# Performance work log

Measured on AMD Instinct MI355X. Metric: run time of the kernel, lower is better.

## Reference

```python
import jax, jax.numpy as jnp
import numpy as np

B, N, E, C_IN, C_OUT = 16, 4096, 131072, 256, 256


def setup_inputs() -> dict:
    key = jax.random.key(0)
    k1, k2, k3, k4 = jax.random.split(key, 4)
    x = jax.random.normal(k1, (B, N, C_IN), dtype=jnp.float32)
    edge_index = jax.random.randint(k2, (B, 2, E), 0, N, dtype=jnp.int32)
    edge_weight = jax.random.uniform(k3, (B, E), dtype=jnp.float32)
    # glorot init for weight [C_in, C_out]
    scale = float(np.sqrt(6.0 / (C_IN + C_OUT)))
    W = jax.random.uniform(k4, (C_IN, C_OUT), dtype=jnp.float32, minval=-scale, maxval=scale)
    return {"x": x, "edge_index": edge_index, "edge_weight": edge_weight, "W": W}


def _gcn_one_graph(xi, ei, ewi, W):
    # xi: [N, C_in], ei: [2, E+N], ewi: [E+N]
    n = xi.shape[0]
    row, col = ei[0], ei[1]
    deg = jax.ops.segment_sum(ewi, row, num_segments=n)            # [N]
    deg_inv = jnp.where(deg > 0, jax.lax.rsqrt(deg), 0.0)          # deg^-0.5, inf -> 0
    norm = deg_inv[row] * ewi * deg_inv[col]                       # [E+N]
    xw = xi @ W                                                    # [N, C_out]
    msg = norm[:, None] * xw[col]                                  # gather + scale
    out = jax.ops.segment_sum(msg, row, num_segments=n)            # scatter-add to rows
    return jax.nn.relu(out)                                        # act = F.relu, bias=False


def reference(x, edge_index, edge_weight, W):
    b, n, _ = x.shape
    # add self loops with weight 1 (fill_value=1)
    loop = jnp.arange(n, dtype=edge_index.dtype)
    loop_idx = jnp.broadcast_to(jnp.stack([loop, loop])[None], (b, 2, n))
    ei = jnp.concatenate([edge_index, loop_idx], axis=-1)          # [B, 2, E+N]
    ew = jnp.concatenate([edge_weight, jnp.ones((b, n), x.dtype)], axis=-1)  # [B, E+N]
    return jax.vmap(_gcn_one_graph, in_axes=(0, 0, 0, None))(x, ei, ew, W)
```

## Files before the change

### kernel.cpp

```cpp
#include <hip/hip_runtime.h>
#include <cstdint>
#include <cstddef>

#define BB 16
#define NN 4096
#define EE 131072
#define CIN 256
#define COUT 256
#define NCH 16
#define CHE (EE / NCH)

typedef __attribute__((ext_vector_type(8))) _Float16 h16x8;
typedef __attribute__((ext_vector_type(4))) float f32x4;

__global__ __launch_bounds__(256) void phaseA_kernel(const float* __restrict__ W, _Float16* __restrict__ wt,
                                                     const int* __restrict__ ei, const float* __restrict__ ew,
                                                     int* __restrict__ chist, float* __restrict__ wdeg) {
    __shared__ int h[NN];
    __shared__ float wh[NN];
    int bid = blockIdx.x;
    int tid = threadIdx.x;
    if (bid < BB * NCH) {
        int b = bid >> 4, c = bid & (NCH - 1);
        for (int i = tid; i < NN; i += 256) { h[i] = 0; wh[i] = 0.f; }
        __syncthreads();
        const int* rows = ei + (size_t)b * 2 * EE + (size_t)c * CHE;
        const float* w = ew + (size_t)b * EE + (size_t)c * CHE;
        #pragma unroll 4
        for (int j = 0; j < CHE / 256; ++j) {
            int row = rows[j * 256 + tid];
            float wv = w[j * 256 + tid];
            atomicAdd(&h[row], 1);
            atomicAdd(&wh[row], wv);
        }
        __syncthreads();
        int* co = chist + ((size_t)b * NCH + c) * NN;
        float* wo = wdeg + ((size_t)b * NCH + c) * NN;
        for (int i = tid; i < NN; i += 256) { co[i] = h[i]; wo[i] = wh[i]; }
    } else {
        int n = bid - BB * NCH;
        int k = tid;
        wt[n * CIN + k] = (_Float16)W[(size_t)k * COUT + n];
    }
}

__global__ __launch_bounds__(1024) void scanfused_kernel(const int* __restrict__ chist, const float* __restrict__ wdeg,
                                                         int* __restrict__ chunkbase, int* __restrict__ roff,
                                                         float* __restrict__ dinv) {
    int b = blockIdx.x, tid = threadIdx.x;
    int wid = tid >> 6, lane = tid & 63;
    __shared__ int wsum[16];
    __shared__ int wbase[16];
    __shared__ int gtot_s;
    int carry = 0;
    for (int g = 0; g < 4; ++g) {
        int r = g * 1024 + tid;
        int cv[NCH];
        int tot = 0;
        float dsum = 1.0f;
        #pragma unroll
        for (int c = 0; c < NCH; ++c) {
            size_t idx = ((size_t)b * NCH + c) * NN + r;
            cv[c] = chist[idx];
            tot += cv[c];
            dsum += wdeg[idx];
        }
        dinv[b * NN + r] = rsqrtf(dsum);
        int incl = tot;
        #pragma unroll
        for (int off = 1; off < 64; off <<= 1) {
            int t = __shfl_up(incl, off, 64);
            if (lane >= off) incl += t;
        }
        if (lane == 63) wsum[wid] = incl;
        __syncthreads();
        if (wid == 0) {
            int v = (lane < 16) ? wsum[lane] : 0;
            int winc = v;
            #pragma unroll
            for (int off = 1; off < 16; off <<= 1) {
                int t = __shfl_up(winc, off, 64);
                if (lane >= off) winc += t;
            }
            if (lane < 16) wbase[lane] = winc - v;
            if (lane == 15) gtot_s = winc;
        }
        __syncthreads();
        int excl = carry + wbase[wid] + (incl - tot);
        roff[b * NN + r] = excl;
        int acc = excl;
        #pragma unroll
        for (int c = 0; c < NCH; ++c) {
            chunkbase[((size_t)b * NCH + c) * NN + r] = acc;
            acc += cv[c];
        }
        carry += gtot_s;
        __syncthreads();
    }
}

__global__ __launch_bounds__(256) void gemm_f32wide_kernel(const float* __restrict__ x, const _Float16* __restrict__ wt,
                                                           _Float16* __restrict__ xw) {
    __shared__ _Float16 As[128 * 64];
    __shared__ _Float16 Bs[256 * 64];
    int tid = threadIdx.x;
    int lane = tid & 63;
    int wave = tid >> 6;
    int row0 = blockIdx.x * 128;
    int wr = wave >> 1, wc = wave & 1;
    int hi = lane >> 4, lo = lane & 15;
    f32x4 acc[4][8] = {};

    for (int kk = 0; kk < CIN; kk += 64) {
        #pragma unroll
        for (int j = 0; j < 4; ++j) {
            int c = j * 256 + tid;
            int r = c >> 3, kq = c & 7;
            const float* g = &x[(size_t)(row0 + r) * CIN + kk + 8 * kq];
            float4 f0 = *reinterpret_cast<const float4*>(g);
            float4 f1 = *reinterpret_cast<const float4*>(g + 4);
            h16x8 v;
            v[0] = (_Float16)f0.x; v[1] = (_Float16)f0.y; v[2] = (_Float16)f0.z; v[3] = (_Float16)f0.w;
            v[4] = (_Float16)f1.x; v[5] = (_Float16)f1.y; v[6] = (_Float16)f1.z; v[7] = (_Float16)f1.w;
            *reinterpret_cast<h16x8*>(&As[r * 64 + 8 * kq]) = v;
        }
        #pragma unroll
        for (int j = 0; j < 8; ++j) {
            int c = j * 256 + tid;
            int r = c >> 3, kq = c & 7;
            *reinterpret_cast<h16x8*>(&Bs[r * 64 + 8 * kq]) =
                *reinterpret_cast<const h16x8*>(&wt[(size_t)r * CIN + kk + 8 * kq]);
        }
        __syncthreads();
        #pragma unroll
        for (int ks = 0; ks < 2; ++ks) {
            h16x8 a[4], b[8];
            #pragma unroll
            for (int m = 0; m < 4; ++m)
                a[m] = *reinterpret_cast<const h16x8*>(&As[(wr * 64 + m * 16 + lo) * 64 + ks * 32 + 8 * hi]);
            #pragma unroll
            for (int n = 0; n < 8; ++n)
                b[n] = *reinterpret_cast<const h16x8*>(&Bs[(wc * 128 + n * 16 + lo) * 64 + ks * 32 + 8 * hi]);
            #pragma unroll
            for (int m = 0; m < 4; ++m)
                #pragma unroll
                for (int n = 0; n < 8; ++n)
                    acc[m][n] = __builtin_amdgcn_mfma_f32_16x16x32_f16(a[m], b[n], acc[m][n], 0, 0, 0);
        }
        __syncthreads();
    }
    #pragma unroll
    for (int m = 0; m < 4; ++m)
        #pragma unroll
        for (int n = 0; n < 8; ++n)
            #pragma unroll
            for (int r = 0; r < 4; ++r) {
                int row = row0 + wr * 64 + m * 16 + hi * 4 + r;
                int col = wc * 128 + n * 16 + lo;
                xw[(size_t)row * COUT + col] = (_Float16)acc[m][n][r];
            }
}

__global__ __launch_bounds__(256) void scatter2_kernel(const int* __restrict__ ei, const float* __restrict__ ew,
                                                       const float* __restrict__ dinv, const int* __restrict__ chunkbase,
                                                       int2* __restrict__ csr) {
    __shared__ int basebuf[NN];
    __shared__ float dinvs[NN];
    int bid = blockIdx.x;
    int xcd = bid & 7;
    int j = bid >> 3;
    int b = xcd * 2 + (j >> 4);
    int c = j & (NCH - 1);
    int tid = threadIdx.x;
    for (int i = tid; i < NN; i += 256) {
        basebuf[i] = chunkbase[((size_t)b * NCH + c) * NN + i];
        dinvs[i] = dinv[b * NN + i];
    }
    __syncthreads();
    const int* rows = ei + (size_t)b * 2 * EE + (size_t)c * CHE;
    const int* cols = rows + EE;
    const float* w = ew + (size_t)b * EE + (size_t)c * CHE;
    int2* cs = csr + (size_t)b * EE;
    #pragma unroll 4
    for (int jj = 0; jj < CHE / 256; ++jj) {
        int e = jj * 256 + tid;
        int row = rows[e];
        int col = cols[e];
        float nm = dinvs[row] * w[e] * dinvs[col];
        int pos = atomicAdd(&basebuf[row], 1);
        int2 pk; pk.x = col * (COUT * 2); pk.y = __float_as_int(nm);
        cs[pos] = pk;
    }
}

#define MIXLO(acc_, w_, nm_) asm("v_fma_mix_f32 %0, %1, %2, %0 op_sel:[0,0,0] op_sel_hi:[1,0,0]" \
                                 : "+v"(acc_) : "v"(w_), "v"(nm_));
#define MIXHI(acc_, w_, nm_) asm("v_fma_mix_f32 %0, %1, %2, %0 op_sel:[1,0,0] op_sel_hi:[1,0,0]" \
                                 : "+v"(acc_) : "v"(w_), "v"(nm_));
#define ACCMIX(w_, nm_) { \
    MIXLO(a0, (w_).x, nm_); MIXHI(a1, (w_).x, nm_); \
    MIXLO(a2, (w_).y, nm_); MIXHI(a3, (w_).y, nm_); \
    MIXLO(a4, (w_).z, nm_); MIXHI(a5, (w_).z, nm_); \
    MIXLO(a6, (w_).w, nm_); MIXHI(a7, (w_).w, nm_); }

__global__ __launch_bounds__(256) void aggregate_kernel(const _Float16* __restrict__ xw, const float* __restrict__ dinv,
                                                        const int* __restrict__ roff, const int2* __restrict__ csr,
                                                        float* __restrict__ out) {
    int bid = blockIdx.x;
    int xcd = bid & 7;
    int idx = bid >> 3;
    int b = xcd * 2 + (idx >> 10);
    int rowblk = idx & 1023;
    int wave = threadIdx.x >> 6;
    int lane = threadIdx.x & 63;
    int n = rowblk * 4 + wave;
    bool hiHalf = lane >= 32;
    int sub = lane & 31;
    int lanebyte = sub * 16;

    const int* rb = roff + b * NN;
    int s = __builtin_amdgcn_readfirstlane(rb[n]);
    int eRaw = (n == NN - 1) ? EE : rb[n + 1];
    int e = __builtin_amdgcn_readfirstlane(eRaw);
    int cnt = e - s;
    const int2* cs = csr + (size_t)b * EE + s;

    const char* xwbase = (const char*)(xw + (size_t)b * NN * COUT);
    float a0 = 0.f, a1 = 0.f, a2 = 0.f, a3 = 0.f, a4 = 0.f, a5 = 0.f, a6 = 0.f, a7 = 0.f;

    {
        float di = dinv[b * NN + n];
        float sn = hiHalf ? 0.f : di * di;
        uint4 w = *reinterpret_cast<const uint4*>(xwbase + (size_t)n * (COUT * 2) + lanebyte);
        ACCMIX(w, sn);
    }

    int m = cnt & ~7;
    int i = 0;
    for (; i < m; i += 8) {
        int2 q[8];
        #pragma unroll
        for (int u = 0; u < 8; ++u) q[u] = cs[i + u];
        #pragma unroll
        for (int u = 0; u < 4; ++u) {
            int offx = (hiHalf ? q[2 * u + 1].x : q[2 * u].x) + lanebyte;
            float nm = __int_as_float(hiHalf ? q[2 * u + 1].y : q[2 * u].y);
            uint4 w = *reinterpret_cast<const uint4*>(xwbase + (uint32_t)offx);
            ACCMIX(w, nm);
        }
    }
    if (i < cnt) {
        #pragma unroll
        for (int u = 0; u < 4; ++u) {
            int j0 = i + 2 * u, j1 = j0 + 1;
            int jc0 = (j0 < cnt) ? j0 : cnt - 1;
            int jc1 = (j1 < cnt) ? j1 : cnt - 1;
            int2 q0 = cs[jc0];
            int2 q1 = cs[jc1];
            int offx = (hiHalf ? q1.x : q0.x) + lanebyte;
            float nm0 = (j0 < cnt) ? __int_as_float(q0.y) : 0.f;
            float nm1 = (j1 < cnt) ? __int_as_float(q1.y) : 0.f;
            float nm = hiHalf ? nm1 : nm0;
            uint4 w = *reinterpret_cast<const uint4*>(xwbase + (uint32_t)offx);
            ACCMIX(w, nm);
        }
    }

    a0 += __shfl(a0, lane ^ 32, 64); a1 += __shfl(a1, lane ^ 32, 64);
    a2 += __shfl(a2, lane ^ 32, 64); a3 += __shfl(a3, lane ^ 32, 64);
    a4 += __shfl(a4, lane ^ 32, 64); a5 += __shfl(a5, lane ^ 32, 64);
    a6 += __shfl(a6, lane ^ 32, 64); a7 += __shfl(a7, lane ^ 32, 64);

    float4 o = hiHalf
        ? make_float4(fmaxf(a4, 0.f), fmaxf(a5, 0.f), fmaxf(a6, 0.f), fmaxf(a7, 0.f))
        : make_float4(fmaxf(a0, 0.f), fmaxf(a1, 0.f), fmaxf(a2, 0.f), fmaxf(a3, 0.f));
    float* orow = out + ((size_t)b * NN + n) * COUT + sub * 8 + (hiHalf ? 4 : 0);
    *reinterpret_cast<float4*>(orow) = o;
}

__global__ __launch_bounds__(256) void cvt_wt_kernel(const float* __restrict__ W, _Float16* __restrict__ wt) {
    int n = blockIdx.x;
    int k = threadIdx.x;
    wt[n * CIN + k] = (_Float16)W[(size_t)k * COUT + n];
}

__global__ __launch_bounds__(256) void init_deg_kernel(float* __restrict__ deg, float v) {
    int i = blockIdx.x * 256 + threadIdx.x;
    if (i < BB * NN) deg[i] = v;
}

__global__ __launch_bounds__(256) void deg_only_kernel(const int* __restrict__ ei, const float* __restrict__ ew,
                                                       float* __restrict__ deg) {
    int idx = blockIdx.x * 256 + threadIdx.x;
    if (idx >= BB * EE) return;
    int b = idx / EE, e = idx - b * EE;
    atomicAdd(&deg[b * NN + ei[(size_t)b * 2 * EE + e]], ew[(size_t)b * EE + e]);
}

__global__ __launch_bounds__(256) void deginv_kernel(const float* __restrict__ deg, float* __restrict__ dinv) {
    int i = blockIdx.x * 256 + threadIdx.x;
    if (i < BB * NN) {
        float d = deg[i];
        dinv[i] = (d > 0.0f) ? rsqrtf(d) : 0.0f;
    }
}

__global__ __launch_bounds__(256) void gemm_f32src_kernel(const float* __restrict__ x, const _Float16* __restrict__ wt,
                                                          _Float16* __restrict__ xw) {
    __shared__ _Float16 As[128][64];
    __shared__ _Float16 Bs[128][64];
    int tid = threadIdx.x;
    int lane = tid & 63;
    int wave = tid >> 6;
    int row0 = blockIdx.x * 128;
    int col0 = blockIdx.y * 128;
    int wr = wave >> 1, wc = wave & 1;
    int hi = lane >> 4, lo = lane & 15;
    f32x4 acc[4][4] = {};
    for (int kk = 0; kk < CIN; kk += 64) {
        #pragma unroll
        for (int j = 0; j < 4; ++j) {
            int c = j * 256 + tid;
            int r = c >> 3, kq = c & 7;
            const float* g = &x[(size_t)(row0 + r) * CIN + kk + 8 * kq];
            float4 f0 = *reinterpret_cast<const float4*>(g);
            float4 f1 = *reinterpret_cast<const float4*>(g + 4);
            h16x8 v;
            v[0] = (_Float16)f0.x; v[1] = (_Float16)f0.y; v[2] = (_Float16)f0.z; v[3] = (_Float16)f0.w;
            v[4] = (_Float16)f1.x; v[5] = (_Float16)f1.y; v[6] = (_Float16)f1.z; v[7] = (_Float16)f1.w;
            *reinterpret_cast<h16x8*>(&As[r][8 * kq]) = v;
        }
        #pragma unroll
        for (int j = 0; j < 4; ++j) {
            int c = j * 256 + tid;
            int r = c >> 3, kq = c & 7;
            *reinterpret_cast<h16x8*>(&Bs[r][8 * kq]) =
                *reinterpret_cast<const h16x8*>(&wt[(size_t)(col0 + r) * CIN + kk + 8 * kq]);
        }
        __syncthreads();
        #pragma unroll
        for (int ks = 0; ks < 2; ++ks) {
            h16x8 a[4], b[4];
            #pragma unroll
            for (int m = 0; m < 4; ++m)
                a[m] = *reinterpret_cast<const h16x8*>(&As[wr * 64 + m * 16 + lo][ks * 32 + 8 * hi]);
            #pragma unroll
            for (int n = 0; n < 4; ++n)
                b[n] = *reinterpret_cast<const h16x8*>(&Bs[wc * 64 + n * 16 + lo][ks * 32 + 8 * hi]);
            #pragma unroll
            for (int m = 0; m < 4; ++m)
                #pragma unroll
                for (int n = 0; n < 4; ++n)
                    acc[m][n] = __builtin_amdgcn_mfma_f32_16x16x32_f16(a[m], b[n], acc[m][n], 0, 0, 0);
        }
        __syncthreads();
    }
    #pragma unroll
    for (int m = 0; m < 4; ++m)
        #pragma unroll
        for (int n = 0; n < 4; ++n)
            #pragma unroll
            for (int r = 0; r < 4; ++r) {
                int row = row0 + wr * 64 + m * 16 + hi * 4 + r;
                int col = col0 + wc * 64 + n * 16 + lo;
                xw[(size_t)row * COUT + col] = (_Float16)acc[m][n][r];
            }
}

__global__ __launch_bounds__(256) void self_kernel(const _Float16* __restrict__ xw, const float* __restrict__ dinv,
                                                   float* __restrict__ out) {
    int bn = blockIdx.x;
    int c = threadIdx.x;
    float di = dinv[bn];
    out[(size_t)bn * COUT + c] = di * di * (float)xw[(size_t)bn * COUT + c];
}

__global__ __launch_bounds__(256) void scatter_atomic_kernel(const int* __restrict__ ei, const float* __restrict__ ew,
                                                             const float* __restrict__ dinv,
                                                             const _Float16* __restrict__ xw, float* __restrict__ out) {
    int be = blockIdx.x;
    int b = be / EE, e = be - b * EE;
    int c = threadIdx.x;
    int row = ei[(size_t)b * 2 * EE + e];
    int col = ei[(size_t)b * 2 * EE + EE + e];
    float w = ew[(size_t)b * EE + e];
    float nm = dinv[b * NN + row] * w * dinv[b * NN + col];
    const _Float16* xwb = xw + (size_t)b * NN * COUT;
    atomicAdd(&out[((size_t)b * NN + row) * COUT + c], nm * (float)xwb[(size_t)col * COUT + c]);
}

__global__ __launch_bounds__(256) void relu_kernel(float* __restrict__ out) {
    size_t i = (size_t)blockIdx.x * 256 + threadIdx.x;
    out[i] = fmaxf(out[i], 0.0f);
}

extern "C" void kernel_launch(void* const* d_in, const int* in_sizes, int n_in,
                              void* d_out, int out_size, void* d_ws, size_t ws_size,
                              hipStream_t stream) {
    const float* x  = (const float*)d_in[0];
    const int*   ei = (const int*)d_in[1];
    const float* ew = (const float*)d_in[2];
    const float* Wm = (const float*)d_in[3];
    float* out = (float*)d_out;

    char* ws = (char*)d_ws;
    size_t off = 0;
    auto alloc = [&](size_t bytes) -> void* {
        void* p = ws + off;
        off += (bytes + 255) & ~(size_t)255;
        return p;
    };
    _Float16* xw        = (_Float16*)alloc((size_t)BB * NN * COUT * 2);
    int2*     csr       = (int2*)alloc((size_t)BB * EE * 8);
    int*      chist     = (int*)alloc((size_t)BB * NCH * NN * 4);
    float*    wdeg      = (float*)alloc((size_t)BB * NCH * NN * 4);
    int*      chunkbase = (int*)alloc((size_t)BB * NCH * NN * 4);
    int*      roff      = (int*)alloc((size_t)BB * NN * 4);
    float*    dinv      = (float*)alloc((size_t)BB * NN * 4);
    _Float16* wt        = (_Float16*)alloc((size_t)CIN * COUT * 2);
    float*    deg_fb    = (float*)chist;
    bool use_csr = (ws_size >= off);

    if (use_csr) {
        phaseA_kernel<<<BB * NCH + COUT, 256, 0, stream>>>(Wm, wt, ei, ew, chist, wdeg);
        scanfused_kernel<<<BB, 1024, 0, stream>>>(chist, wdeg, chunkbase, roff, dinv);
        gemm_f32wide_kernel<<<BB * NN / 128, 256, 0, stream>>>(x, wt, xw);
        scatter2_kernel<<<BB * NCH, 256, 0, stream>>>(ei, ew, dinv, chunkbase, csr);
        aggregate_kernel<<<BB * NN / 4, 256, 0, stream>>>(xw, dinv, roff, csr, out);
    } else {
        const int bnBlocks = (BB * NN) / 256;
        cvt_wt_kernel<<<COUT, CIN, 0, stream>>>(Wm, wt);
        init_deg_kernel<<<bnBlocks, 256, 0, stream>>>(deg_fb, 1.0f);
        deg_only_kernel<<<(BB * EE) / 256, 256, 0, stream>>>(ei, ew, deg_fb);
        deginv_kernel<<<bnBlocks, 256, 0, stream>>>(deg_fb, dinv);
        dim3 ggrid((BB * NN) / 128, COUT / 128);
        gemm_f32src_kernel<<<ggrid, 256, 0, stream>>>(x, wt, xw);
        self_kernel<<<BB * NN, 256, 0, stream>>>(xw, dinv, out);
        scatter_atomic_kernel<<<BB * EE, 256, 0, stream>>>(ei, ew, dinv, xw, out);
        relu_kernel<<<(BB * NN * COUT) / 256, 256, 0, stream>>>(out);
    }
}
```

Measured before the change: 139.9 us.

## Merge GEMM and CSR scatter into one launch to overlap them

New measurement: 137.2 us. Within noise of the previous version (-2.0%).

```diff
diff --git a/kernel.cpp b/kernel.cpp
--- a/kernel.cpp
+++ b/kernel.cpp
@@ -12,6 +12,8 @@
 
 typedef __attribute__((ext_vector_type(8))) _Float16 h16x8;
 typedef __attribute__((ext_vector_type(4))) float f32x4;
+
+#define PKRTZ(a, b) __builtin_bit_cast(uint32_t, __builtin_amdgcn_cvt_pkrtz((a), (b)))
 
 __global__ __launch_bounds__(256) void phaseA_kernel(const float* __restrict__ W, _Float16* __restrict__ wt,
                                                      const int* __restrict__ ei, const float* __restrict__ ew,
@@ -99,97 +101,98 @@
     }
 }
 
-__global__ __launch_bounds__(256) void gemm_f32wide_kernel(const float* __restrict__ x, const _Float16* __restrict__ wt,
-                                                           _Float16* __restrict__ xw) {
-    __shared__ _Float16 As[128 * 64];
-    __shared__ _Float16 Bs[256 * 64];
+__global__ __launch_bounds__(256) void gemm_scatter_kernel(const float* __restrict__ x, const _Float16* __restrict__ wt,
+                                                           _Float16* __restrict__ xw,
+                                                           const int* __restrict__ ei, const float* __restrict__ ew,
+                                                           const float* __restrict__ dinv, const int* __restrict__ chunkbase,
+                                                           int2* __restrict__ csr) {
+    __shared__ __align__(16) char smem[49152];
+    int bid = blockIdx.x;
     int tid = threadIdx.x;
-    int lane = tid & 63;
-    int wave = tid >> 6;
-    int row0 = blockIdx.x * 128;
-    int wr = wave >> 1, wc = wave & 1;
-    int hi = lane >> 4, lo = lane & 15;
-    f32x4 acc[4][8] = {};
-
-    for (int kk = 0; kk < CIN; kk += 64) {
-        #pragma unroll
-        for (int j = 0; j < 4; ++j) {
-            int c = j * 256 + tid;
-            int r = c >> 3, kq = c & 7;
-            const float* g = &x[(size_t)(row0 + r) * CIN + kk + 8 * kq];
-            float4 f0 = *reinterpret_cast<const float4*>(g);
-            float4 f1 = *reinterpret_cast<const float4*>(g + 4);
-            h16x8 v;
-            v[0] = (_Float16)f0.x; v[1] = (_Float16)f0.y; v[2] = (_Float16)f0.z; v[3] = (_Float16)f0.w;
-            v[4] = (_Float16)f1.x; v[5] = (_Float16)f1.y; v[6] = (_Float16)f1.z; v[7] = (_Float16)f1.w;
-            *reinterpret_cast<h16x8*>(&As[r * 64 + 8 * kq]) = v;
-        }
-        #pragma unroll
-        for (int j = 0; j < 8; ++j) {
-            int c = j * 256 + tid;
-            int r = c >> 3, kq = c & 7;
-            *reinterpret_cast<h16x8*>(&Bs[r * 64 + 8 * kq]) =
-                *reinterpret_cast<const h16x8*>(&wt[(size_t)r * CIN + kk + 8 * kq]);
-        }
-        __syncthreads();
-        #pragma unroll
-        for (int ks = 0; ks < 2; ++ks) {
-            h16x8 a[4], b[8];
-            #pragma unroll
-            for (int m = 0; m < 4; ++m)
-                a[m] = *reinterpret_cast<const h16x8*>(&As[(wr * 64 + m * 16 + lo) * 64 + ks * 32 + 8 * hi]);
-            #pragma unroll
-            for (int n = 0; n < 8; ++n)
-                b[n] = *reinterpret_cast<const h16x8*>(&Bs[(wc * 128 + n * 16 + lo) * 64 + ks * 32 + 8 * hi]);
-            #pragma unroll
-            for (int m = 0; m < 4; ++m)
+    if (bid < 256) {
+        int* basebuf = (int*)smem;
+        float* dinvs = (float*)(smem + 16384);
+        int b = bid >> 4, c = bid & (NCH - 1);
+        for (int i = tid; i < NN; i += 256) {
+            basebuf[i] = chunkbase[((size_t)b * NCH + c) * NN + i];
+            dinvs[i] = dinv[b * NN + i];
+        }
+        __syncthreads();
+        const int* rows = ei + (size_t)b * 2 * EE + (size_t)c * CHE;
+        const int* cols = rows + EE;
+        const float* w = ew + (size_t)b * EE + (size_t)c * CHE;
+        int2* cs = csr + (size_t)b * EE;
+        #pragma unroll 4
+        for (int jj = 0; jj < CHE / 256; ++jj) {
+            int e = jj * 256 + tid;
+            int row = rows[e];
+            int col = cols[e];
+            float nm = dinvs[row] * w[e] * dinvs[col];
+            int pos = atomicAdd(&basebuf[row], 1);
+            int2 pk; pk.x = col * (COUT * 2); pk.y = __float_as_int(nm);
+            cs[pos] = pk;
+        }
+    } else {
+        _Float16* As = (_Float16*)smem;
+        _Float16* Bs = As + 128 * 64;
+        int g = bid - 256;
+        int lane = tid & 63;
+        int wave = tid >> 6;
+        int row0 = g * 128;
+        int wr = wave >> 1, wc = wave & 1;
+        int hi = lane >> 4, lo = lane & 15;
+        f32x4 acc[4][8] = {};
+
+        for (int kk = 0; kk < CIN; kk += 64) {
+            #pragma unroll
+            for (int j = 0; j < 4; ++j) {
+                int c = j * 256 + tid;
+                int r = c >> 3, kq = c & 7;
+                const float* gp = &x[(size_t)(row0 + r) * CIN + kk + 8 * kq];
+                float4 f0 = *reinterpret_cast<const float4*>(gp);
+                float4 f1 = *reinterpret_cast<const float4*>(gp + 4);
+                uint4 v;
+                v.x = PKRTZ(f0.x, f0.y);
+                v.y = PKRTZ(f0.z, f0.w);
+                v.z = PKRTZ(f1.x, f1.y);
+                v.w = PKRTZ(f1.z, f1.w);
+                *reinterpret_cast<uint4*>(&As[r * 64 + 8 * kq]) = v;
+            }
+            #pragma unroll
+            for (int j = 0; j < 8; ++j) {
+                int c = j * 256 + tid;
+                int r = c >> 3, kq = c & 7;
+                *reinterpret_cast<h16x8*>(&Bs[r * 64 + 8 * kq]) =
+                    *reinterpret_cast<const h16x8*>(&wt[(size_t)r * CIN + kk + 8 * kq]);
+            }
+            __syncthreads();
+            #pragma unroll
+            for (int ks = 0; ks < 2; ++ks) {
+                h16x8 a[4], b[8];
+                #pragma unroll
+                for (int m = 0; m < 4; ++m)
+                    a[m] = *reinterpret_cast<const h16x8*>(&As[(wr * 64 + m * 16 + lo) * 64 + ks * 32 + 8 * hi]);
                 #pragma unroll
                 for (int n = 0; n < 8; ++n)
-                    acc[m][n] = __builtin_amdgcn_mfma_f32_16x16x32_f16(a[m], b[n], acc[m][n], 0, 0, 0);
-        }
-        __syncthreads();
-    }
-    #pragma unroll
-    for (int m = 0; m < 4; ++m)
-        #pragma unroll
-        for (int n = 0; n < 8; ++n)
-            #pragma unroll
-            for (int r = 0; r < 4; ++r) {
-                int row = row0 + wr * 64 + m * 16 + hi * 4 + r;
-                int col = wc * 128 + n * 16 + lo;
-                xw[(size_t)row * COUT + col] = (_Float16)acc[m][n][r];
+                    b[n] = *reinterpret_cast<const h16x8*>(&Bs[(wc * 128 + n * 16 + lo) * 64 + ks * 32 + 8 * hi]);
+                #pragma unroll
+                for (int m = 0; m < 4; ++m)
+                    #pragma unroll
+                    for (int n = 0; n < 8; ++n)
+                        acc[m][n] = __builtin_amdgcn_mfma_f32_16x16x32_f16(a[m], b[n], acc[m][n], 0, 0, 0);
             }
-}
-
-__global__ __launch_bounds__(256) void scatter2_kernel(const int* __restrict__ ei, const float* __restrict__ ew,
-                                                       const float* __restrict__ dinv, const int* __restrict__ chunkbase,
-                                                       int2* __restrict__ csr) {
-    __shared__ int basebuf[NN];
-    __shared__ float dinvs[NN];
-    int bid = blockIdx.x;
-    int xcd = bid & 7;
-    int j = bid >> 3;
-    int b = xcd * 2 + (j >> 4);
-    int c = j & (NCH - 1);
-    int tid = threadIdx.x;
-    for (int i = tid; i < NN; i += 256) {
-        basebuf[i] = chunkbase[((size_t)b * NCH + c) * NN + i];
-        dinvs[i] = dinv[b * NN + i];
-    }
-    __syncthreads();
-    const int* rows = ei + (size_t)b * 2 * EE + (size_t)c * CHE;
-    const int* cols = rows + EE;
-    const float* w = ew + (size_t)b * EE + (size_t)c * CHE;
-    int2* cs = csr + (size_t)b * EE;
-    #pragma unroll 4
-    for (int jj = 0; jj < CHE / 256; ++jj) {
-        int e = jj * 256 + tid;
-        int row = rows[e];
-        int col = cols[e];
-        float nm = dinvs[row] * w[e] * dinvs[col];
-        int pos = atomicAdd(&basebuf[row], 1);
-        int2 pk; pk.x = col * (COUT * 2); pk.y = __float_as_int(nm);
-        cs[pos] = pk;
+            __syncthreads();
+        }
+        #pragma unroll
+        for (int m = 0; m < 4; ++m)
+            #pragma unroll
+            for (int n = 0; n < 8; ++n)
+                #pragma unroll
+                for (int r = 0; r < 4; ++r) {
+                    int row = row0 + wr * 64 + m * 16 + hi * 4 + r;
+                    int col = wc * 128 + n * 16 + lo;
+                    xw[(size_t)row * COUT + col] = (_Float16)acc[m][n][r];
+                }
     }
 }
 
@@ -424,8 +427,7 @@
     if (use_csr) {
         phaseA_kernel<<<BB * NCH + COUT, 256, 0, stream>>>(Wm, wt, ei, ew, chist, wdeg);
         scanfused_kernel<<<BB, 1024, 0, stream>>>(chist, wdeg, chunkbase, roff, dinv);
-        gemm_f32wide_kernel<<<BB * NN / 128, 256, 0, stream>>>(x, wt, xw);
-        scatter2_kernel<<<BB * NCH, 256, 0, stream>>>(ei, ew, dinv, chunkbase, csr);
+        gemm_scatter_kernel<<<256 + BB * NN / 128, 256, 0, stream>>>(x, wt, xw, ei, ew, dinv, chunkbase, csr);
         aggregate_kernel<<<BB * NN / 4, 256, 0, stream>>>(xw, dinv, roff, csr, out);
     } else {
         const int bnBlocks = (BB * NN) / 256;
```
